# Performance work log

Measured on AMD Instinct MI355X. Metric: run time of the kernel, lower is better.

Reference implementation:

```python
import jax, jax.numpy as jnp
import numpy as np

NSIDE = 64
LMAX = 96
MMAX = 96
NLAT = 4 * NSIDE - 1
B, C = 4, 64


def healpix_nlon_ring(t, nside):
    if 0 <= t < nside - 1:
        return 4 * (t + 1)
    if t <= 3 * nside - 1:
        return 4 * nside
    return 4 * (4 * nside - t - 1)


NLON = [healpix_nlon_ring(t, NSIDE) for t in range(NLAT)]


def healpix_latitude_theta(nside):
    t = np.arange(0, 4 * nside - 1).astype(np.float64)
    z = np.zeros_like(t)
    m1 = t < nside - 1
    m2 = (t >= nside - 1) & (t <= 3 * nside - 1)
    m3 = (t > 3 * nside - 1) & (t <= 4 * nside - 2)
    z[m1] = 1 - (t[m1] + 1) ** 2 / (3 * nside ** 2)
    z[m2] = 4 / 3 - 2 * (t[m2] + 1) / (3 * nside)
    z[m3] = (4 * nside - 1 - t[m3]) ** 2 / (3 * nside ** 2) - 1
    return np.arccos(z)


def healpix_longitude_offset(mmax, nside):
    t = np.arange(0, 4 * nside - 1).astype(np.float64)
    shift = 0.5
    tt = np.zeros_like(t)
    tt = np.where((t + 1 >= nside) & (t + 1 <= 3 * nside), shift * ((t - nside + 2) % 2) * np.pi / (2 * nside), tt)
    tt = np.where(t + 1 > 3 * nside, shift * np.pi / (2 * (4 * nside - t - 1)), tt)
    tt = np.where(t + 1 < nside, shift * np.pi / (2 * (t + 1)), tt)
    return np.einsum('t,m->tm', tt, np.arange(0, mmax).astype(np.float64))


def legpoly(mmax, lmax, x, norm='ortho', inverse=False, csphase=True):
    # (-1)^m c^l_m P^l_m(x), shape (mmax, lmax, len(x)); faithful numpy copy
    nmax = max(mmax, lmax)
    vdm = np.zeros((nmax, nmax, len(x)), dtype=np.float64)
    norm_factor = 1.0 if norm == 'ortho' else np.sqrt(4 * np.pi)
    norm_factor = 1.0 / norm_factor if inverse else norm_factor
    vdm[0, 0, :] = norm_factor / np.sqrt(4 * np.pi)
    for n in range(1, nmax):
        vdm[n - 1, n, :] = np.sqrt(2 * n + 1) * x * vdm[n - 1, n - 1, :]
        vdm[n, n, :] = np.sqrt((2 * n + 1) * (1 + x) * (1 - x) / 2 / n) * vdm[n - 1, n - 1, :]
    for n in range(2, nmax):
        for m in range(0, n - 1):
            vdm[m, n, :] = (x * np.sqrt((2 * n - 1) / (n - m) * (2 * n + 1) / (n + m)) * vdm[m, n - 1, :]
                            - np.sqrt((n + m - 1) / (n - m) * (2 * n + 1) / (2 * n - 3) * (n - m - 1) / (n + m)) * vdm[m, n - 2, :])
    if norm == 'schmidt':
        for num in range(0, nmax):
            if inverse:
                vdm[:, num, :] = vdm[:, num, :] * np.sqrt(2 * num + 1)
            else:
                vdm[:, num, :] = vdm[:, num, :] / np.sqrt(2 * num + 1)
    vdm = vdm[:mmax, :lmax]
    if csphase:
        vdm[1::2] *= -1
    return vdm


def setup_inputs() -> dict:
    key = jax.random.key(0)
    k1, k2 = jax.random.split(key)
    x_real = jax.random.normal(k1, (B, C, LMAX, MMAX), dtype=jnp.float32)
    x_imag = jax.random.normal(k2, (B, C, LMAX, MMAX), dtype=jnp.float32)
    theta = healpix_latitude_theta(NSIDE)
    pct = legpoly(MMAX, LMAX, np.cos(theta), norm='ortho', inverse=True, csphase=True)  # (M, L, NLAT)
    offset = healpix_longitude_offset(MMAX, NSIDE)  # (NLAT, M)
    return {
        'x_real': x_real,
        'x_imag': x_imag,
        'pct': jnp.asarray(pct, dtype=jnp.float32),
        'offset': jnp.asarray(offset, dtype=jnp.float32),
    }


def reference(x_real, x_imag, pct, offset):
    # Legendre transform: (..., l, m) x (m, l, k) -> (..., k=nlat, m)
    rl = jnp.einsum('...lm,mlk->...km', x_real, pct)
    im = jnp.einsum('...lm,mlk->...km', x_imag, pct)
    x = (rl + 1j * im) * jnp.exp(1j * offset)  # (..., NLAT, MMAX) complex64
    # ragged per-ring irfft: group rings sharing the same nlon into one batched irfft
    groups = {}
    for t, n in enumerate(NLON):
        groups.setdefault(n, []).append(t)
    ring_out = [None] * NLAT
    for n, idxs in groups.items():
        y = jnp.fft.irfft(x[..., jnp.asarray(idxs), :], n=n, axis=-1, norm='forward')  # (..., g, n)
        for i, t in enumerate(idxs):
            ring_out[t] = y[..., i, :]
    return jnp.concatenate(ring_out, axis=-1)  # (..., 12*nside^2)
```

## Files before the change

kernel.cpp:

```cpp
#include <hip/hip_runtime.h>
#include <hip/hip_bf16.h>
#include <math.h>

#define NLAT 255
#define NPIX 49152
#define PI_F 3.14159265358979323846f

typedef _Float16 half_t;
typedef half_t half8 __attribute__((ext_vector_type(8)));
typedef float  f32x4 __attribute__((ext_vector_type(4)));

__device__ __forceinline__ void ring_params(int t, int& n, int& roff) {
    if (t < 63)        { n = 4 * (t + 1); roff = 2 * t * (t + 1); }
    else if (t <= 191) { n = 256;         roff = 8064 + 256 * (t - 63); }
    else               { int w = 255 - t; n = 4 * w; roff = 49152 - 2 * w * (w + 1); }
}

__global__ __launch_bounds__(256) void k_prep(
        const float* __restrict__ pct,
        const float* __restrict__ xr, const float* __restrict__ xi,
        half_t* __restrict__ pctT, half_t* __restrict__ xh,
        half_t* __restrict__ W) {
    __shared__ float smem[96 * 33];
    const int bx  = blockIdx.x;
    const int tid = threadIdx.x;

    if (bx < 768) {
        const int m = bx >> 3, t0 = (bx & 7) * 32;
        for (int idx = tid; idx < 96 * 32; idx += 256) {
            int l = idx >> 5, tt = idx & 31, t = t0 + tt;
            smem[l * 33 + tt] = (t < NLAT) ? pct[((size_t)m * 96 + l) * NLAT + t] : 0.f;
        }
        __syncthreads();
        for (int idx = tid; idx < 96 * 32; idx += 256) {
            int tt = idx / 96, l = idx - tt * 96;
            pctT[((size_t)m * 256 + t0 + tt) * 96 + l] = (half_t)smem[l * 33 + tt];
        }
    } else if (bx < 5376) {
        const int id  = bx - 768;
        const int z   = id / 768;
        const int rem = id - z * 768;
        const int l   = rem % 96;
        const int bc0 = (rem / 96) * 32;
        const int comp = z / 3, m0 = (z % 3) * 32;
        const float* in = comp ? xi : xr;
        const int tx = tid & 31, ty = tid >> 5;
#pragma unroll
        for (int j = 0; j < 4; ++j) {
            int bcl = ty + j * 8;
            smem[bcl * 33 + tx] = in[((size_t)(bc0 + bcl) * 96 + l) * 96 + m0 + tx];
        }
        __syncthreads();
#pragma unroll
        for (int j = 0; j < 4; ++j) {
            int ml = ty + j * 8;
            xh[((((size_t)(comp * 96 + m0 + ml)) * 12 + (l >> 3)) * 256 + bc0 + tx) * 8
               + (l & 7)] = (half_t)smem[tx * 33 + ml];
        }
    } else {
        int gid   = (bx - 5376) * 256 + tid;
        int chunk = gid & 31;
        int pix   = gid >> 5;
        if (chunk >= 24 || pix >= NPIX) return;

        int t, p;
        if (pix < 8064) {
            int tt = (int)((sqrtf((float)(2 * pix + 1)) - 1.0f) * 0.5f);
            while (2 * tt * (tt + 1) > pix) --tt;
            while (2 * (tt + 1) * (tt + 2) <= pix) ++tt;
            t = tt; p = pix - 2 * tt * (tt + 1);
        } else if (pix < 41088) {
            t = 63 + ((pix - 8064) >> 8); p = (pix - 8064) & 255;
        } else {
            int r = NPIX - 1 - pix;
            int tt = (int)((sqrtf((float)(2 * r + 1)) - 1.0f) * 0.5f);
            while (2 * tt * (tt + 1) > r) --tt;
            while (2 * (tt + 1) * (tt + 2) <= r) ++tt;
            int w = tt + 1;
            t = 254 - tt;
            p = pix - (NPIX - 2 * w * (w + 1));
        }
        int n, roff; ring_params(t, n, roff);
        const int n2 = n >> 1;
        float alpha = (t < 63)   ? PI_F / (4.0f * (float)(t + 1))
                    : (t <= 191) ? (((t - 62) & 1) ? PI_F / 256.0f : 0.0f)
                    :              PI_F / (4.0f * (float)(255 - t));
        float phi = 6.28318530717958647692f * (float)p / (float)n + alpha;

        int m0 = chunk * 4;
        float c, s, cd, sd;
        __sincosf((float)m0 * phi, &s, &c);
        __sincosf(phi, &sd, &cd);
        half8 v;
#pragma unroll
        for (int j = 0; j < 4; ++j) {
            int m = m0 + j;
            float sc = (m == 0) ? 1.f : (m < n2) ? 2.f : (m == n2) ? 1.f : 0.f;
            v[2 * j]     = (half_t)(sc * c);
            v[2 * j + 1] = (half_t)(-sc * s);
            float cn = c * cd - s * sd; s = s * cd + c * sd; c = cn;
        }
        *(half8*)(W + (size_t)pix * 192 + chunk * 8) = v;
    }
}

__global__ __launch_bounds__(256) void k_leg(
        const half_t* __restrict__ pctT, const half_t* __restrict__ xh,
        half_t* __restrict__ Xp) {
    const int mg  = blockIdx.x;
    const int t0  = blockIdx.y * 64;
    const int bc0 = blockIdx.z * 32;
    const int wid = threadIdx.x >> 6, lane = threadIdx.x & 63;
    const int wm = wid & 1, wn = wid >> 1;
    const int row = lane & 15, quad = lane >> 4;
    const int tbase = t0 + wm * 32;
    const int bc    = bc0 + wn * 16 + row;

    f32x4 acc[4][2][2];
#pragma unroll
    for (int a = 0; a < 4; ++a)
#pragma unroll
        for (int b = 0; b < 2; ++b)
#pragma unroll
            for (int d = 0; d < 2; ++d) acc[a][b][d] = (f32x4)0.f;

#pragma unroll
    for (int k0 = 0; k0 < 96; k0 += 32) {
        const int kA = k0 + quad * 8;
        half8 af[4][2], bf[4][2];
#pragma unroll
        for (int mi = 0; mi < 4; ++mi) {
            const int m = mg * 4 + mi;
#pragma unroll
            for (int mt = 0; mt < 2; ++mt)
                af[mi][mt] = *(const half8*)(pctT +
                    ((size_t)m * 256 + tbase + mt * 16 + row) * 96 + kA);
#pragma unroll
            for (int c = 0; c < 2; ++c)
                bf[mi][c] = *(const half8*)(xh +
                    ((((size_t)(c * 96 + m)) * 12 + (k0 >> 3) + quad) * 256 + bc) * 8);
        }
#pragma unroll
        for (int mi = 0; mi < 4; ++mi)
#pragma unroll
            for (int c = 0; c < 2; ++c)
#pragma unroll
                for (int mt = 0; mt < 2; ++mt)
                    acc[mi][c][mt] = __builtin_amdgcn_mfma_f32_16x16x32_f16(
                        af[mi][mt], bf[mi][c], acc[mi][c][mt], 0, 0, 0);
    }

#pragma unroll
    for (int mt = 0; mt < 2; ++mt)
#pragma unroll
        for (int r = 0; r < 4; ++r) {
            const int t = tbase + mt * 16 + quad * 4 + r;
            half8 v;
#pragma unroll
            for (int mi = 0; mi < 4; ++mi) {
                v[2 * mi]     = (half_t)acc[mi][0][mt][r];
                v[2 * mi + 1] = (half_t)acc[mi][1][mt][r];
            }
            *(half8*)(Xp + (((size_t)t * 24 + mg) * 256 + bc) * 8) = v;
        }
}

__device__ __forceinline__ void dft_step(int kk,
        const half_t* __restrict__ wb, const half_t* __restrict__ xpb,
        f32x4 acc[4][4]) {
    half8 a[4], b[4];
#pragma unroll
    for (int bn = 0; bn < 4; ++bn)
        b[bn] = *(const half8*)(xpb + kk * 8192 + bn * 128);
#pragma unroll
    for (int pi = 0; pi < 4; ++pi)
        a[pi] = *(const half8*)(wb + kk * 32 + pi * 3072);
#pragma unroll
    for (int pi = 0; pi < 4; ++pi)
#pragma unroll
        for (int bn = 0; bn < 4; ++bn)
            acc[pi][bn] = __builtin_amdgcn_mfma_f32_16x16x32_f16(
                a[pi], b[bn], acc[pi][bn], 0, 0, 0);
}

__global__ __launch_bounds__(256) void k_dft(
        const half_t* __restrict__ W, const half_t* __restrict__ Xp,
        float* __restrict__ out) {
    const int bid = blockIdx.x;
    const int xcd = bid & 7, sub = bid >> 3;
    const int wg  = (xcd < 4 ? xcd * 128 : 512 + (xcd - 4) * 127) + sub;
    const int t   = wg >> 2;
    const int p0  = (wg & 3) * 64;
    int n, roff; ring_params(t, n, roff);
    if (p0 >= n) return;

    const int wid = threadIdx.x >> 6, lane = threadIdx.x & 63;
    const int row = lane & 15, quad = lane >> 4;

    const half_t* wb  = W  + (size_t)(roff + p0 + row) * 192 + quad * 8;
    const half_t* xpb = Xp + (((size_t)t * 24 + quad) * 256 + wid * 64 + row) * 8;

    const int mh = min(95, n >> 1);
    const int ks = (2 * (mh + 1) + 31) >> 5;

    f32x4 acc[4][4];
#pragma unroll
    for (int i = 0; i < 4; ++i)
#pragma unroll
        for (int j = 0; j < 4; ++j) acc[i][j] = (f32x4)0.f;

    if (ks == 6) {
#pragma unroll
        for (int kk = 0; kk < 6; ++kk) dft_step(kk, wb, xpb, acc);
    } else {
        for (int kk = 0; kk < ks; ++kk) dft_step(kk, wb, xpb, acc);
    }

#pragma unroll
    for (int pi = 0; pi < 4; ++pi) {
        const int p = p0 + pi * 16 + quad * 4;
        if (p < n) {
#pragma unroll
            for (int bn = 0; bn < 4; ++bn) {
                const int bc = wid * 64 + bn * 16 + row;
                float4 v = make_float4(acc[pi][bn][0], acc[pi][bn][1],
                                       acc[pi][bn][2], acc[pi][bn][3]);
                *(float4*)(out + (size_t)bc * NPIX + roff + p) = v;
            }
        }
    }
}

extern "C" void kernel_launch(void* const* d_in, const int* in_sizes, int n_in,
                              void* d_out, int out_size, void* d_ws, size_t ws_size,
                              hipStream_t stream) {
    const float* xr  = (const float*)d_in[0];
    const float* xi  = (const float*)d_in[1];
    const float* pct = (const float*)d_in[2];
    float* out = (float*)d_out;

    char* ws = (char*)d_ws;
    half_t* W    = (half_t*)ws;
    half_t* pctT = (half_t*)(ws + 18923520);
    half_t* xh   = (half_t*)(ws + 18923520 + 4718592);
    half_t* Xp   = (half_t*)(ws + 18923520 + 4718592 + 9437184);

    k_prep<<<dim3(11520), 256, 0, stream>>>(pct, xr, xi, pctT, xh, W);
    k_leg <<<dim3(24, 4, 8), 256, 0, stream>>>(pctT, xh, Xp);
    k_dft <<<dim3(1020), 256, 0, stream>>>(W, Xp, out);
}
```

Measured before the change: 142.8 us.

## Generate DFT twiddle factors on the fly in k_dft instead of precomputing W

Removes the precomputed twiddle matrix W (about 19 MB of fp16 written in k_prep and read back in k_dft). Each lane of k_dft now derives its cos/sin values with a few sincos calls and a complex rotation recurrence per k-step, so the global write and read traffic for W goes away. In exchange the DFT kernel does extra ALU work and register use before each group of MFMAs. The long rotation chains may also lose some accuracy compared with direct sincos.

```diff
diff --git a/kernel.cpp b/kernel.cpp
--- a/kernel.cpp
+++ b/kernel.cpp
@@ -16,11 +16,16 @@
     else               { int w = 255 - t; n = 4 * w; roff = 49152 - 2 * w * (w + 1); }
 }
 
+__device__ __forceinline__ float ring_alpha(int t) {
+    return (t < 63)   ? PI_F / (4.0f * (float)(t + 1))
+         : (t <= 191) ? ((((t - 62) & 1)) ? PI_F / 256.0f : 0.0f)
+         :              PI_F / (4.0f * (float)(255 - t));
+}
+
 __global__ __launch_bounds__(256) void k_prep(
         const float* __restrict__ pct,
         const float* __restrict__ xr, const float* __restrict__ xi,
-        half_t* __restrict__ pctT, half_t* __restrict__ xh,
-        half_t* __restrict__ W) {
+        half_t* __restrict__ pctT, half_t* __restrict__ xh) {
     __shared__ float smem[96 * 33];
     const int bx  = blockIdx.x;
     const int tid = threadIdx.x;
@@ -36,7 +41,7 @@
             int tt = idx / 96, l = idx - tt * 96;
             pctT[((size_t)m * 256 + t0 + tt) * 96 + l] = (half_t)smem[l * 33 + tt];
         }
-    } else if (bx < 5376) {
+    } else {
         const int id  = bx - 768;
         const int z   = id / 768;
         const int rem = id - z * 768;
@@ -57,50 +62,6 @@
             xh[((((size_t)(comp * 96 + m0 + ml)) * 12 + (l >> 3)) * 256 + bc0 + tx) * 8
                + (l & 7)] = (half_t)smem[tx * 33 + ml];
         }
-    } else {
-        int gid   = (bx - 5376) * 256 + tid;
-        int chunk = gid & 31;
-        int pix   = gid >> 5;
-        if (chunk >= 24 || pix >= NPIX) return;
-
-        int t, p;
-        if (pix < 8064) {
-            int tt = (int)((sqrtf((float)(2 * pix + 1)) - 1.0f) * 0.5f);
-            while (2 * tt * (tt + 1) > pix) --tt;
-            while (2 * (tt + 1) * (tt + 2) <= pix) ++tt;
-            t = tt; p = pix - 2 * tt * (tt + 1);
-        } else if (pix < 41088) {
-            t = 63 + ((pix - 8064) >> 8); p = (pix - 8064) & 255;
-        } else {
-            int r = NPIX - 1 - pix;
-            int tt = (int)((sqrtf((float)(2 * r + 1)) - 1.0f) * 0.5f);
-            while (2 * tt * (tt + 1) > r) --tt;
-            while (2 * (tt + 1) * (tt + 2) <= r) ++tt;
-            int w = tt + 1;
-            t = 254 - tt;
-            p = pix - (NPIX - 2 * w * (w + 1));
-        }
-        int n, roff; ring_params(t, n, roff);
-        const int n2 = n >> 1;
-        float alpha = (t < 63)   ? PI_F / (4.0f * (float)(t + 1))
-                    : (t <= 191) ? (((t - 62) & 1) ? PI_F / 256.0f : 0.0f)
-                    :              PI_F / (4.0f * (float)(255 - t));
-        float phi = 6.28318530717958647692f * (float)p / (float)n + alpha;
-
-        int m0 = chunk * 4;
-        float c, s, cd, sd;
-        __sincosf((float)m0 * phi, &s, &c);
-        __sincosf(phi, &sd, &cd);
-        half8 v;
-#pragma unroll
-        for (int j = 0; j < 4; ++j) {
-            int m = m0 + j;
-            float sc = (m == 0) ? 1.f : (m < n2) ? 2.f : (m == n2) ? 1.f : 0.f;
-            v[2 * j]     = (half_t)(sc * c);
-            v[2 * j + 1] = (half_t)(-sc * s);
-            float cn = c * cd - s * sd; s = s * cd + c * sd; c = cn;
-        }
-        *(half8*)(W + (size_t)pix * 192 + chunk * 8) = v;
     }
 }
 
@@ -165,27 +126,8 @@
         }
 }
 
-__device__ __forceinline__ void dft_step(int kk,
-        const half_t* __restrict__ wb, const half_t* __restrict__ xpb,
-        f32x4 acc[4][4]) {
-    half8 a[4], b[4];
-#pragma unroll
-    for (int bn = 0; bn < 4; ++bn)
-        b[bn] = *(const half8*)(xpb + kk * 8192 + bn * 128);
-#pragma unroll
-    for (int pi = 0; pi < 4; ++pi)
-        a[pi] = *(const half8*)(wb + kk * 32 + pi * 3072);
-#pragma unroll
-    for (int pi = 0; pi < 4; ++pi)
-#pragma unroll
-        for (int bn = 0; bn < 4; ++bn)
-            acc[pi][bn] = __builtin_amdgcn_mfma_f32_16x16x32_f16(
-                a[pi], b[bn], acc[pi][bn], 0, 0, 0);
-}
-
 __global__ __launch_bounds__(256) void k_dft(
-        const half_t* __restrict__ W, const half_t* __restrict__ Xp,
-        float* __restrict__ out) {
+        const half_t* __restrict__ Xp, float* __restrict__ out) {
     const int bid = blockIdx.x;
     const int xcd = bid & 7, sub = bid >> 3;
     const int wg  = (xcd < 4 ? xcd * 128 : 512 + (xcd - 4) * 127) + sub;
@@ -196,24 +138,70 @@
 
     const int wid = threadIdx.x >> 6, lane = threadIdx.x & 63;
     const int row = lane & 15, quad = lane >> 4;
-
-    const half_t* wb  = W  + (size_t)(roff + p0 + row) * 192 + quad * 8;
+    const int mq  = quad * 4;
+
     const half_t* xpb = Xp + (((size_t)t * 24 + quad) * 256 + wid * 64 + row) * 8;
 
-    const int mh = min(95, n >> 1);
+    const int n2 = n >> 1;
+    const int mh = min(95, n2);
     const int ks = (2 * (mh + 1) + 31) >> 5;
 
+    const float alpha = ring_alpha(t);
+    const float invn  = 1.0f / (float)n;
+    float cc[4], ss[4], d1c[4], d1s[4], d16c[4], d16s[4];
+#pragma unroll
+    for (int pi = 0; pi < 4; ++pi) {
+        float phi = 6.28318530717958647692f * (float)(p0 + pi * 16 + row) * invn
+                  + alpha;
+        __sincosf(phi, &d1s[pi], &d1c[pi]);
+        __sincosf(16.0f * phi, &d16s[pi], &d16c[pi]);
+        __sincosf((float)mq * phi, &ss[pi], &cc[pi]);
+    }
+
     f32x4 acc[4][4];
 #pragma unroll
     for (int i = 0; i < 4; ++i)
 #pragma unroll
         for (int j = 0; j < 4; ++j) acc[i][j] = (f32x4)0.f;
 
+    auto step = [&](int kk) {
+        half8 b[4];
+#pragma unroll
+        for (int bn = 0; bn < 4; ++bn)
+            b[bn] = *(const half8*)(xpb + kk * 8192 + bn * 128);
+        half8 af[4];
+#pragma unroll
+        for (int pi = 0; pi < 4; ++pi) {
+            float c = cc[pi], s = ss[pi];
+            half8 a;
+#pragma unroll
+            for (int j = 0; j < 4; ++j) {
+                int m = kk * 16 + mq + j;
+                float sc = (m == 0) ? 1.f : (m < n2) ? 2.f : (m == n2) ? 1.f : 0.f;
+                a[2 * j]     = (half_t)(sc * c);
+                a[2 * j + 1] = (half_t)(-sc * s);
+                float cn = c * d1c[pi] - s * d1s[pi];
+                s = s * d1c[pi] + c * d1s[pi];
+                c = cn;
+            }
+            float cn = cc[pi] * d16c[pi] - ss[pi] * d16s[pi];
+            ss[pi] = ss[pi] * d16c[pi] + cc[pi] * d16s[pi];
+            cc[pi] = cn;
+            af[pi] = a;
+        }
+#pragma unroll
+        for (int pi = 0; pi < 4; ++pi)
+#pragma unroll
+            for (int bn = 0; bn < 4; ++bn)
+                acc[pi][bn] = __builtin_amdgcn_mfma_f32_16x16x32_f16(
+                    af[pi], b[bn], acc[pi][bn], 0, 0, 0);
+    };
+
     if (ks == 6) {
 #pragma unroll
-        for (int kk = 0; kk < 6; ++kk) dft_step(kk, wb, xpb, acc);
+        for (int kk = 0; kk < 6; ++kk) step(kk);
     } else {
-        for (int kk = 0; kk < ks; ++kk) dft_step(kk, wb, xpb, acc);
+        for (int kk = 0; kk < ks; ++kk) step(kk);
     }
 
 #pragma unroll
@@ -240,12 +228,11 @@
     float* out = (float*)d_out;
 
     char* ws = (char*)d_ws;
-    half_t* W    = (half_t*)ws;
-    half_t* pctT = (half_t*)(ws + 18923520);
-    half_t* xh   = (half_t*)(ws + 18923520 + 4718592);
-    half_t* Xp   = (half_t*)(ws + 18923520 + 4718592 + 9437184);
-
-    k_prep<<<dim3(11520), 256, 0, stream>>>(pct, xr, xi, pctT, xh, W);
+    half_t* pctT = (half_t*)ws;
+    half_t* xh   = (half_t*)(ws + 4718592);
+    half_t* Xp   = (half_t*)(ws + 4718592 + 9437184);
+
+    k_prep<<<dim3(5376), 256, 0, stream>>>(pct, xr, xi, pctT, xh);
     k_leg <<<dim3(24, 4, 8), 256, 0, stream>>>(pctT, xh, Xp);
-    k_dft <<<dim3(1020), 256, 0, stream>>>(W, Xp, out);
-}
+    k_dft <<<dim3(1020), 256, 0, stream>>>(Xp, out);
+}
```

After: 136.5 us. 1.05x faster.
